# Kernel optimization log

Measured on AMD Instinct MI355X. Metric: run time of the kernel, lower is better.

The kernel has to match this reference:

```python
import jax, jax.numpy as jnp
import numpy as np

B, N, C, K = 4, 4096, 128, 16
LN_EPS = 1e-5


def knn(x, k):
    # x: [B,N,3] -> idx of k nearest (incl. self): [B,N,k]
    xx = jnp.sum(x * x, axis=2, keepdims=True)            # [B,N,1]
    inner = -2.0 * jnp.matmul(x, jnp.swapaxes(x, 1, 2))   # [B,N,N]
    pairwise = -xx - inner - jnp.swapaxes(xx, 1, 2)       # = -||xi-xj||^2
    _, idx = jax.lax.top_k(pairwise, k)                   # largest = nearest
    return idx


def index_points(points, idx):
    # points: [B,N,C], idx: [B,N,K] -> [B,N,K,C]
    return jax.vmap(lambda p, i: p[i])(points, idx)


def layer_norm(x, g, b):
    m = jnp.mean(x, axis=-1, keepdims=True)
    v = jnp.mean((x - m) ** 2, axis=-1, keepdims=True)
    return (x - m) * jax.lax.rsqrt(v + LN_EPS) * g + b


def setup_inputs() -> dict:
    key = jax.random.key(0)
    ks = jax.random.split(key, 16)
    h, q = C // 2, C // 4
    w = lambda k, s, sc: jax.random.normal(k, s, jnp.float32) * sc
    return dict(
        xyz=jax.random.normal(ks[0], (B, N, 3), jnp.float32),
        features=jax.random.normal(ks[1], (B, N, C), jnp.float32),
        geo_w1=w(ks[2], (10, h), 0.3), geo_b1=jnp.zeros((h,), jnp.float32),
        geo_g1=jnp.ones((h,), jnp.float32), geo_be1=jnp.zeros((h,), jnp.float32),
        geo_w2=w(ks[3], (h, h), 0.12), geo_b2=jnp.zeros((h,), jnp.float32),
        diff_w1=w(ks[4], (C, h), 0.09), diff_b1=jnp.zeros((h,), jnp.float32),
        diff_g1=jnp.ones((h,), jnp.float32), diff_be1=jnp.zeros((h,), jnp.float32),
        diff_w2=w(ks[5], (h, h), 0.12), diff_b2=jnp.zeros((h,), jnp.float32),
        ep_w1=w(ks[6], (C, q), 0.09), ep_b1=jnp.zeros((q,), jnp.float32),
        ep_w2=w(ks[7], (q, 1), 0.17), ep_b2=jnp.zeros((1,), jnp.float32),
        ref_w1=w(ks[8], (2 * C, C), 0.06), ref_b1=jnp.zeros((C,), jnp.float32),
        ref_g1=jnp.ones((C,), jnp.float32), ref_be1=jnp.zeros((C,), jnp.float32),
    )


def reference(xyz, features,
              geo_w1, geo_b1, geo_g1, geo_be1, geo_w2, geo_b2,
              diff_w1, diff_b1, diff_g1, diff_be1, diff_w2, diff_b2,
              ep_w1, ep_b1, ep_w2, ep_b2,
              ref_w1, ref_b1, ref_g1, ref_be1):
    # --- geometric features ---
    idx = knn(xyz, K)                                    # [B,N,K]
    neighbors = index_points(xyz, idx)                   # [B,N,K,3]
    rel_pos = neighbors - xyz[:, :, None, :]             # [B,N,K,3]
    cov = jnp.einsum('bnkc,bnkd->bncd', rel_pos, rel_pos) / K  # [B,N,3,3]
    _, eigvecs = jnp.linalg.eigh(cov)                    # ascending eigenvalues
    normal = eigvecs[..., :, 0]                          # smallest-eig direction
    curvature_dir = eigvecs[..., :, 2]                   # largest-eig direction
    mean_rel = jnp.mean(rel_pos, axis=2)                 # [B,N,3]
    mean_dist = jnp.mean(jnp.linalg.norm(rel_pos, axis=-1), axis=-1, keepdims=True)
    geo_feat = jnp.concatenate([normal, curvature_dir, mean_rel, mean_dist], axis=-1)  # [B,N,10]

    geo_h = layer_norm(geo_feat @ geo_w1 + geo_b1, geo_g1, geo_be1)
    geo_encoded = jax.nn.relu(geo_h) @ geo_w2 + geo_b2   # [B,N,C/2]

    # --- feature differences (knn recomputed as in the original) ---
    idx2 = knn(xyz, K)
    neighbor_feats = index_points(features, idx2)        # [B,N,K,C]
    feat_diff = jnp.mean(jnp.abs(features[:, :, None, :] - neighbor_feats), axis=2)  # [B,N,C]
    diff_h = layer_norm(feat_diff @ diff_w1 + diff_b1, diff_g1, diff_be1)
    diff_encoded = jax.nn.relu(diff_h) @ diff_w2 + diff_b2

    # --- edge probability + refinement ---
    edge_feat = jnp.concatenate([geo_encoded, diff_encoded], axis=-1)  # [B,N,C]
    ep_h = jax.nn.relu(edge_feat @ ep_w1 + ep_b1)
    edge_prob = jax.nn.sigmoid(ep_h @ ep_w2 + ep_b2)     # [B,N,1]

    enhanced = jnp.concatenate([features, edge_feat * edge_prob], axis=-1)  # [B,N,2C]
    refined = jax.nn.relu(layer_norm(enhanced @ ref_w1 + ref_b1, ref_g1, ref_be1))
    refined = refined + features                          # dropout in eval mode = identity
    return refined, edge_prob
```

## Files before the change

### kernel.cpp

```cpp
#include <hip/hip_runtime.h>
#include <hip/hip_bf16.h>

#define N_ 4096
#define C_ 128
#define K_ 16
#define NPT 16384

__device__ __forceinline__ float wave_sum64(float v) {
#pragma unroll
  for (int off = 32; off >= 1; off >>= 1) v += __shfl_xor(v, off, 64);
  return v;
}


__device__ __forceinline__ float sign_f(float a, float b) {
  return copysignf(fabsf(a), b);
}

__device__ float lapy2_f(float x, float y) {
#pragma clang fp contract(off)
  float xa = fabsf(x), ya = fabsf(y);
  float w = fmaxf(xa, ya), z = fminf(xa, ya);
  if (z == 0.0f) return w;
  float t = z / w;
  return w * sqrtf(1.0f + t * t);
}

__device__ void lartg_f(float f, float g, float& c, float& s, float& r) {
#pragma clang fp contract(off)
  if (g == 0.0f) {
    c = 1.0f; s = 0.0f; r = f;
  } else if (f == 0.0f) {
    c = 0.0f; s = copysignf(1.0f, g); r = fabsf(g);
  } else {
    float d = sqrtf(f * f + g * g);
    c = fabsf(f) / d;
    r = sign_f(d, f);
    s = g / r;
  }
}

__device__ void laev2_f(float a, float b, float cc, float& rt1, float& rt2,
                        float& cs1, float& sn1) {
#pragma clang fp contract(off)
  float sm = a + cc;
  float df = a - cc;
  float adf = fabsf(df);
  float tb = b + b;
  float ab = fabsf(tb);
  float acmx, acmn;
  if (fabsf(a) > fabsf(cc)) { acmx = a; acmn = cc; } else { acmx = cc; acmn = a; }
  float rt;
  if (adf > ab) {
    float t = ab / adf; rt = adf * sqrtf(1.0f + t * t);
  } else if (adf < ab) {
    float t = adf / ab; rt = ab * sqrtf(1.0f + t * t);
  } else {
    rt = ab * sqrtf(2.0f);
  }
  int sgn1;
  if (sm < 0.0f) {
    rt1 = 0.5f * (sm - rt); sgn1 = -1;
    rt2 = (acmx / rt1) * acmn - (b / rt1) * b;
  } else if (sm > 0.0f) {
    rt1 = 0.5f * (sm + rt); sgn1 = 1;
    rt2 = (acmx / rt1) * acmn - (b / rt1) * b;
  } else {
    rt1 = 0.5f * rt; rt2 = -0.5f * rt; sgn1 = 1;
  }
  float cs; int sgn2;
  if (df >= 0.0f) { cs = df + rt; sgn2 = 1; } else { cs = df - rt; sgn2 = -1; }
  float acs = fabsf(cs);
  if (acs > ab) {
    float ct = -tb / cs;
    sn1 = 1.0f / sqrtf(1.0f + ct * ct);
    cs1 = ct * sn1;
  } else {
    if (ab == 0.0f) { cs1 = 1.0f; sn1 = 0.0f; }
    else {
      float tn = -cs / tb;
      cs1 = 1.0f / sqrtf(1.0f + tn * tn);
      sn1 = tn * cs1;
    }
  }
  if (sgn1 == sgn2) { float tn = cs1; cs1 = -sn1; sn1 = tn; }
}

__device__ void steqr3_f(float d[3], float e[2], float Z[3][3]) {
#pragma clang fp contract(off)
  const int n = 3;
  const float eps = 5.9604644775390625e-08f;
  const float eps2 = eps * eps;
  const float safmin = 1.17549435e-38f;
  const int nmaxit = n * 30;
  int jtot = 0;
  int l1 = 1;

  for (int og = 0; og < 16; ++og) {
    if (l1 > n) break;
    if (l1 > 1) e[l1 - 2] = 0.0f;
    int m, l, lend;
    if (l1 <= n - 1) {
      bool found = false;
      for (m = l1; m <= n - 1; ++m) {
        float tst = fabsf(e[m - 1]);
        if (tst == 0.0f) { found = true; break; }
        if (tst <= (sqrtf(fabsf(d[m - 1])) * sqrtf(fabsf(d[m]))) * eps) {
          e[m - 1] = 0.0f; found = true; break;
        }
      }
      if (!found) m = n;
    } else {
      m = n;
    }
    l = l1; lend = m; l1 = m + 1;
    if (lend == l) continue;
    if (fabsf(d[lend - 1]) < fabsf(d[l - 1])) { int t = l; l = lend; lend = t; }

    if (lend > l) {
      for (int it = 0; it < 128; ++it) {
        int mm;
        if (l != lend) {
          bool f2 = false;
          for (mm = l; mm <= lend - 1; ++mm) {
            float tst = e[mm - 1] * e[mm - 1];
            if (tst <= (eps2 * fabsf(d[mm - 1])) * fabsf(d[mm]) + safmin) { f2 = true; break; }
          }
          if (!f2) mm = lend;
        } else mm = lend;
        if (mm < lend) e[mm - 1] = 0.0f;
        float p = d[l - 1];
        if (mm == l) {
          d[l - 1] = p; ++l;
          if (l <= lend) continue;
          break;
        }
        if (mm == l + 1) {
          float rt1, rt2, cc, ss;
          laev2_f(d[l - 1], e[l - 1], d[l], rt1, rt2, cc, ss);
          for (int r = 0; r < n; ++r) {
            float temp = Z[r][l];
            Z[r][l] = cc * temp - ss * Z[r][l - 1];
            Z[r][l - 1] = ss * temp + cc * Z[r][l - 1];
          }
          d[l - 1] = rt1; d[l] = rt2; e[l - 1] = 0.0f;
          l += 2;
          if (l <= lend) continue;
          break;
        }
        if (jtot == nmaxit) break;
        ++jtot;
        float g = (d[l] - p) / (2.0f * e[l - 1]);
        float r = lapy2_f(g, 1.0f);
        g = d[mm - 1] - p + e[l - 1] / (g + sign_f(r, g));
        float s = 1.0f, c = 1.0f;
        p = 0.0f;
        float csv[2], snv[2];
        for (int i = mm - 1; i >= l; --i) {
          float f = s * e[i - 1];
          float bb = c * e[i - 1];
          lartg_f(g, f, c, s, r);
          if (i != mm - 1) e[i] = r;
          g = d[i] - p;
          r = (d[i - 1] - g) * s + 2.0f * c * bb;
          p = s * r;
          d[i] = g + p;
          g = c * r - bb;
          csv[i - l] = c;
          snv[i - l] = -s;
        }
        int mml = mm - l;
        for (int j = mml; j >= 1; --j) {
          float cc = csv[j - 1], ss = snv[j - 1];
          for (int r2 = 0; r2 < n; ++r2) {
            float temp = Z[r2][l + j - 1];
            Z[r2][l + j - 1] = cc * temp - ss * Z[r2][l + j - 2];
            Z[r2][l + j - 2] = ss * temp + cc * Z[r2][l + j - 2];
          }
        }
        d[l - 1] -= p;
        e[l - 1] = g;
      }
    } else {
      for (int it = 0; it < 128; ++it) {
        int mm;
        if (l != lend) {
          bool f2 = false;
          for (mm = l; mm >= lend + 1; --mm) {
            float tst = e[mm - 2] * e[mm - 2];
            if (tst <= (eps2 * fabsf(d[mm - 1])) * fabsf(d[mm - 2]) + safmin) { f2 = true; break; }
          }
          if (!f2) mm = lend;
        } else mm = lend;
        if (mm > lend) e[mm - 2] = 0.0f;
        float p = d[l - 1];
        if (mm == l) {
          d[l - 1] = p; --l;
          if (l >= lend) continue;
          break;
        }
        if (mm == l - 1) {
          float rt1, rt2, cc, ss;
          laev2_f(d[l - 2], e[l - 2], d[l - 1], rt1, rt2, cc, ss);
          for (int r = 0; r < n; ++r) {
            float temp = Z[r][l - 1];
            Z[r][l - 1] = cc * temp - ss * Z[r][l - 2];
            Z[r][l - 2] = ss * temp + cc * Z[r][l - 2];
          }
          d[l - 2] = rt1; d[l - 1] = rt2; e[l - 2] = 0.0f;
          l -= 2;
          if (l >= lend) continue;
          break;
        }
        if (jtot == nmaxit) break;
        ++jtot;
        float g = (d[l - 2] - p) / (2.0f * e[l - 2]);
        float r = lapy2_f(g, 1.0f);
        g = d[mm - 1] - p + e[l - 2] / (g + sign_f(r, g));
        float s = 1.0f, c = 1.0f;
        p = 0.0f;
        float csv[2], snv[2];
        for (int i = mm; i <= l - 1; ++i) {
          float f = s * e[i - 1];
          float bb = c * e[i - 1];
          lartg_f(g, f, c, s, r);
          if (i != mm) e[i - 2] = r;
          g = d[i - 1] - p;
          r = (d[i] - g) * s + 2.0f * c * bb;
          p = s * r;
          d[i - 1] = g + p;
          g = c * r - bb;
          csv[i - mm] = c;
          snv[i - mm] = s;
        }
        int lm = l - mm;
        for (int j = 1; j <= lm; ++j) {
          float cc = csv[j - 1], ss = snv[j - 1];
          for (int r2 = 0; r2 < n; ++r2) {
            float temp = Z[r2][mm + j - 1];
            Z[r2][mm + j - 1] = cc * temp - ss * Z[r2][mm + j - 2];
            Z[r2][mm + j - 2] = ss * temp + cc * Z[r2][mm + j - 2];
          }
        }
        d[l - 1] -= p;
        e[l - 2] = g;
      }
    }
  }
  for (int ii = 2; ii <= n; ++ii) {
    int i = ii - 1, k = i;
    float p = d[i - 1];
    for (int j = ii; j <= n; ++j) {
      if (d[j - 1] < p) { k = j; p = d[j - 1]; }
    }
    if (k != i) {
      d[k - 1] = d[i - 1]; d[i - 1] = p;
      for (int r = 0; r < n; ++r) {
        float t = Z[r][i - 1]; Z[r][i - 1] = Z[r][k - 1]; Z[r][k - 1] = t;
      }
    }
  }
}

__device__ void eig3_f(float A00, float A10, float A20,
                       float A11, float A21, float A22, float Z[3][3]) {
#pragma clang fp contract(off)
  float d[3], e[2];
  float tau = 0.0f, v2 = 0.0f;
  d[0] = A00;
  float xnorm = fabsf(A20);
  if (xnorm == 0.0f) {
    tau = 0.0f; v2 = 0.0f;
    e[0] = A10; d[1] = A11; e[1] = A21; d[2] = A22;
  } else {
    float beta = -sign_f(lapy2_f(A10, xnorm), A10);
    tau = (beta - A10) / beta;
    float inv = 1.0f / (A10 - beta);
    v2 = A20 * inv;
    e[0] = beta;
    float x0 = tau * A11;
    float x1 = tau * A21;
    float tmp2 = A21 * v2;
    x0 = x0 + tau * tmp2;
    x1 = x1 + (tau * v2) * A22;
    float dotv = x0 + x1 * v2;
    float aw = (-0.5f * tau) * dotv;
    float w0 = x0 + aw;
    float w1 = x1 + aw * v2;
    d[1] = (A11 - w0) - w0;
    float pq = v2 * w0;
    e[1] = (A21 - pq) - w1;
    float pr = v2 * w1;
    d[2] = (A22 - pr) - pr;
  }
  Z[0][0] = 1.0f; Z[0][1] = 0.0f; Z[0][2] = 0.0f;
  Z[1][0] = 0.0f; Z[1][1] = 1.0f; Z[1][2] = 0.0f;
  Z[2][0] = 0.0f; Z[2][1] = 0.0f; Z[2][2] = 1.0f;
  steqr3_f(d, e, Z);
  if (tau != 0.0f) {
    for (int j = 0; j < 3; ++j) {
      float sum = Z[1][j] + v2 * Z[2][j];
      float tw = tau * sum;
      Z[1][j] = Z[1][j] - tw;
      Z[2][j] = Z[2][j] - v2 * tw;
    }
  }
}

__device__ __forceinline__ unsigned long long knn_key(float qx, float qy, float qz,
                                                      float nqxx, float x, float y,
                                                      float z, int j) {
  const float dot = __fmaf_rn(qz, z, __fmaf_rn(qy, y, __fmul_rn(qx, x)));
  const float xxj =
      __fadd_rn(__fadd_rn(__fmul_rn(x, x), __fmul_rn(y, y)), __fmul_rn(z, z));
  const float inner = __fmul_rn(-2.0f, dot);
  const float pval = __fsub_rn(__fsub_rn(nqxx, inner), xxj);
  const unsigned bits = __float_as_uint(pval);
  const unsigned ordv = bits ^ (unsigned)(((int)bits >> 31) | 0x80000000);
  return ((unsigned long long)ordv << 32) | (unsigned)(4095 - j);
}

__global__ __launch_bounds__(256, 6) void knn_kernel(const float* __restrict__ xyz,
                                                     int* __restrict__ nidx_ws) {
  __shared__ float4 tile4[1024];

  const int wave = threadIdx.x >> 6;
  const int lane = threadIdx.x & 63;
  const int tid = threadIdx.x;
  const int P0 = blockIdx.x * 8;
  const int b = P0 >> 12;
  const int r0 = P0 & 4095;
  const int pbase = r0 + wave * 2;
  const float* xb = xyz + (size_t)b * (N_ * 3);

  float qx[2], qy[2], qz[2], nqxx[2];
#pragma unroll
  for (int q = 0; q < 2; ++q) {
    const int i = pbase + q;
    qx[q] = xb[3 * i]; qy[q] = xb[3 * i + 1]; qz[q] = xb[3 * i + 2];
    nqxx[q] = -__fadd_rn(__fadd_rn(__fmul_rn(qx[q], qx[q]), __fmul_rn(qy[q], qy[q])),
                         __fmul_rn(qz[q], qz[q]));
  }

  unsigned long long pk[2][4];
#pragma unroll
  for (int q = 0; q < 2; ++q)
#pragma unroll
    for (int s = 0; s < 4; ++s) pk[q][s] = 0ull;

  for (int tile = 0; tile < 4; ++tile) {
    {
      const float4* gsrc = (const float4*)(xb + tile * 3072);
      float4 a0 = gsrc[tid * 3];
      float4 a1 = gsrc[tid * 3 + 1];
      float4 a2 = gsrc[tid * 3 + 2];
      const int base = tid * 4;
      tile4[base]     = make_float4(a0.x, a0.y, a0.z, 0.0f);
      tile4[base + 1] = make_float4(a0.w, a1.x, a1.y, 0.0f);
      tile4[base + 2] = make_float4(a1.z, a1.w, a2.x, 0.0f);
      tile4[base + 3] = make_float4(a2.y, a2.z, a2.w, 0.0f);
    }
    __syncthreads();

#pragma unroll 2
    for (int tloc = 0; tloc < 16; ++tloc) {
      const int idx = tloc * 64 + lane;
      const int j = tile * 1024 + idx;
      const float4 pv = tile4[idx];
      const float x = pv.x;
      const float y = pv.y;
      const float z = pv.z;
      const float xxj =
          __fadd_rn(__fadd_rn(__fmul_rn(x, x), __fmul_rn(y, y)), __fmul_rn(z, z));
      const unsigned jenc = (unsigned)(4095 - j);
#pragma unroll
      for (int q = 0; q < 2; ++q) {
        const float dot =
            __fmaf_rn(qz[q], z, __fmaf_rn(qy[q], y, __fmul_rn(qx[q], x)));
        const float inner = __fmul_rn(-2.0f, dot);
        const float pval = __fsub_rn(__fsub_rn(nqxx[q], inner), xxj);
        const unsigned bits = __float_as_uint(pval);
        const unsigned ordv = bits ^ (unsigned)(((int)bits >> 31) | 0x80000000);
        const unsigned long long key = ((unsigned long long)ordv << 32) | jenc;
        const bool c3 = key > pk[q][3];
        if (__any(c3)) {
          const bool c0 = key > pk[q][0], c1 = key > pk[q][1], c2 = key > pk[q][2];
          pk[q][3] = c3 ? (c2 ? pk[q][2] : key) : pk[q][3];
          pk[q][2] = c2 ? (c1 ? pk[q][1] : key) : pk[q][2];
          pk[q][1] = c1 ? (c0 ? pk[q][0] : key) : pk[q][1];
          pk[q][0] = c0 ? key : pk[q][0];
        }
      }
    }
    __syncthreads();
  }

  int stash[2];
  int h[2] = {0, 0};
#pragma unroll
  for (int k = 0; k < K_; ++k) {
    unsigned long long v[2];
#pragma unroll
    for (int q = 0; q < 2; ++q) v[q] = pk[q][0];
#pragma unroll
    for (int off = 32; off >= 1; off >>= 1) {
#pragma unroll
      for (int q = 0; q < 2; ++q) {
        unsigned long long ov = __shfl_xor(v[q], off, 64);
        if (ov > v[q]) v[q] = ov;
      }
    }
#pragma unroll
    for (int q = 0; q < 2; ++q) {
      const int jidx = (4095 - (int)(unsigned)(v[q] & 0xFFFFFFFFull)) & (N_ - 1);
      if (lane == k) stash[q] = jidx;
      if (pk[q][0] == v[q]) {
        pk[q][0] = pk[q][1]; pk[q][1] = pk[q][2]; pk[q][2] = pk[q][3];
        pk[q][3] = 0ull;
        ++h[q];
      }
    }
  }
#pragma unroll
  for (int q = 0; q < 2; ++q) {
    if (__ballot(h[q] >= 4) != 0ull) {
      unsigned long long qq[K_];
#pragma unroll
      for (int k = 0; k < K_; ++k) qq[k] = 0ull;
      for (int t = 0; t < 64; ++t) {
        const int j = t * 64 + lane;
        const unsigned long long key = knn_key(qx[q], qy[q], qz[q], nqxx[q],
                                               xb[3 * j], xb[3 * j + 1],
                                               xb[3 * j + 2], j);
        bool c[K_];
#pragma unroll
        for (int s = 0; s < K_; ++s) c[s] = key > qq[s];
#pragma unroll
        for (int s = K_ - 1; s >= 1; --s)
          qq[s] = c[s] ? (c[s - 1] ? qq[s - 1] : key) : qq[s];
        qq[0] = c[0] ? key : qq[0];
      }
#pragma unroll
      for (int k = 0; k < K_; ++k) {
        unsigned long long v = qq[0];
#pragma unroll
        for (int off = 32; off >= 1; off >>= 1) {
          unsigned long long ov = __shfl_xor(v, off, 64);
          if (ov > v) v = ov;
        }
        const int jidx = (4095 - (int)(unsigned)(v & 0xFFFFFFFFull)) & (N_ - 1);
        if (lane == k) stash[q] = jidx;
        if (qq[0] == v) {
#pragma unroll
          for (int s = 0; s < K_ - 1; ++s) qq[s] = qq[s + 1];
          qq[K_ - 1] = 0ull;
        }
      }
    }
  }

  if (lane < K_) {
    const int pg = P0 + wave * 2;
#pragma unroll
    for (int q = 0; q < 2; ++q)
      nidx_ws[(size_t)(pg + q) * K_ + lane] = stash[q];
  }
}

__global__ __launch_bounds__(64) void eig_kernel(const float* __restrict__ xyz,
                                                 const int* __restrict__ nidx_ws,
                                                 float* __restrict__ gf_ws) {
  const int p = blockIdx.x * 64 + threadIdx.x;
  const int b = p >> 12;
  const int i = p & 4095;
  const float* xb = xyz + (size_t)b * (N_ * 3);
  const float qx = xb[3 * i];
  const float qy = xb[3 * i + 1];
  const float qz = xb[3 * i + 2];

  int nidx[K_];
#pragma unroll
  for (int k = 0; k < K_; ++k) nidx[k] = nidx_ws[(size_t)p * K_ + k];

  float c00 = 0, c01 = 0, c02 = 0, c11 = 0, c12 = 0, c22 = 0;
  float mrx = 0, mry = 0, mrz = 0, md = 0;
#pragma unroll
  for (int k = 0; k < K_; ++k) {
    const int j = nidx[k];
    const float rx = __fsub_rn(xb[3 * j], qx);
    const float ry = __fsub_rn(xb[3 * j + 1], qy);
    const float rz = __fsub_rn(xb[3 * j + 2], qz);
    c00 = __fadd_rn(c00, __fmul_rn(rx, rx));
    c01 = __fadd_rn(c01, __fmul_rn(rx, ry));
    c02 = __fadd_rn(c02, __fmul_rn(rx, rz));
    c11 = __fadd_rn(c11, __fmul_rn(ry, ry));
    c12 = __fadd_rn(c12, __fmul_rn(ry, rz));
    c22 = __fadd_rn(c22, __fmul_rn(rz, rz));
    mrx = __fadd_rn(mrx, rx);
    mry = __fadd_rn(mry, ry);
    mrz = __fadd_rn(mrz, rz);
    const float nn = __fadd_rn(__fadd_rn(__fmul_rn(rx, rx), __fmul_rn(ry, ry)),
                               __fmul_rn(rz, rz));
    md = __fadd_rn(md, sqrtf(nn));
  }
  const float s16 = 0.0625f;
  float Z[3][3];
  eig3_f(__fmul_rn(c00, s16), __fmul_rn(c01, s16), __fmul_rn(c02, s16),
         __fmul_rn(c11, s16), __fmul_rn(c12, s16), __fmul_rn(c22, s16), Z);
  float* g = gf_ws + (size_t)p * 12;
  g[0] = Z[0][0]; g[1] = Z[1][0]; g[2] = Z[2][0];
  g[3] = Z[0][2]; g[4] = Z[1][2]; g[5] = Z[2][2];
  g[6] = __fmul_rn(mrx, s16); g[7] = __fmul_rn(mry, s16);
  g[8] = __fmul_rn(mrz, s16);
  g[9] = __fmul_rn(md, s16);
}

__global__ __launch_bounds__(256) void mlp_kernel(
    const float* __restrict__ feats, const int* __restrict__ nidx_ws,
    const float* __restrict__ gf_ws,
    const float* __restrict__ geo_w1, const float* __restrict__ geo_b1,
    const float* __restrict__ geo_g1, const float* __restrict__ geo_be1,
    const float* __restrict__ geo_w2, const float* __restrict__ geo_b2,
    const float* __restrict__ diff_w1, const float* __restrict__ diff_b1,
    const float* __restrict__ diff_g1, const float* __restrict__ diff_be1,
    const float* __restrict__ diff_w2, const float* __restrict__ diff_b2,
    const float* __restrict__ ep_w1, const float* __restrict__ ep_b1,
    const float* __restrict__ ep_w2, const float* __restrict__ ep_b2,
    const float* __restrict__ ref_w1, const float* __restrict__ ref_b1,
    const float* __restrict__ ref_g1, const float* __restrict__ ref_be1,
    float* __restrict__ out, float* __restrict__ out_prob) {

  __shared__ float w[8192];
  __shared__ float fsh[16 * 128];
  __shared__ float sdif[16 * 128];
  __shared__ float ysh[16 * 64];
  __shared__ float edsh[16 * 128];
  __shared__ float insh[16 * 12];
  __shared__ int nsh[16 * 16];

  const int tid = threadIdx.x;
  const int lane = tid & 63;
  const int g = tid >> 6;
  const int P0 = blockIdx.x * 16;
  const int b = P0 >> 12;
  const int r0 = P0 & 4095;
  const float* fb = feats + (size_t)b * N_ * C_;

  if (tid < 192) insh[tid] = gf_ws[(size_t)P0 * 12 + tid];
  nsh[tid] = nidx_ws[(size_t)P0 * K_ + tid];
#pragma unroll
  for (int m = 0; m < 8; ++m)
    fsh[m * 256 + tid] = fb[(size_t)r0 * C_ + m * 256 + tid];
  if (tid < 160) ((float4*)w)[tid] = ((const float4*)geo_w1)[tid];
#pragma unroll
  for (int m = 0; m < 4; ++m)
    ((float4*)(w + 640))[m * 256 + tid] = ((const float4*)geo_w2)[m * 256 + tid];
  __syncthreads();

  {
    float acc[4] = {0, 0, 0, 0};
#pragma unroll
    for (int c = 0; c < 10; ++c) {
      const float wv = w[c * 64 + lane];
#pragma unroll
      for (int ptl = 0; ptl < 4; ++ptl)
        acc[ptl] += insh[(g * 4 + ptl) * 12 + c] * wv;
    }
#pragma unroll
    for (int ptl = 0; ptl < 4; ++ptl) {
      const int pt = g * 4 + ptl;
      float a = acc[ptl] + geo_b1[lane];
      float m = wave_sum64(a) * (1.0f / 64.0f);
      float xm = a - m;
      float var = wave_sum64(xm * xm) * (1.0f / 64.0f);
      float yv = xm * (1.0f / sqrtf(var + 1e-5f)) * geo_g1[lane] + geo_be1[lane];
      ysh[pt * 64 + lane] = fmaxf(yv, 0.0f);
    }
  }
  __syncthreads();

  float ge[4] = {0, 0, 0, 0}, de[4], prob[4];
#pragma unroll 4
  for (int c = 0; c < 64; ++c) {
    const float wv = w[640 + c * 64 + lane];
#pragma unroll
    for (int ptl = 0; ptl < 4; ++ptl)
      ge[ptl] += ysh[(g * 4 + ptl) * 64 + c] * wv;
  }
#pragma unroll
  for (int ptl = 0; ptl < 4; ++ptl) ge[ptl] += geo_b2[lane];

  {
    const int h2 = tid >> 7, c = tid & 127;
    for (int ptp = 0; ptp < 8; ++ptp) {
      const int pt = h2 * 8 + ptp;
      const float fv = fsh[pt * 128 + c];
      float s = 0.0f;
#pragma unroll
      for (int k = 0; k < K_; ++k) {
        const int j = nsh[pt * 16 + k];
        s += fabsf(fv - fb[(size_t)j * C_ + c]);
      }
      sdif[pt * 128 + c] = s * (1.0f / 16.0f);
    }
  }
  __syncthreads();
#pragma unroll
  for (int m = 0; m < 8; ++m)
    ((float4*)w)[m * 256 + tid] = ((const float4*)diff_w1)[m * 256 + tid];
  __syncthreads();

  {
    float acc[4] = {0, 0, 0, 0};
#pragma unroll 4
    for (int c = 0; c < 128; ++c) {
      const float wv = w[c * 64 + lane];
#pragma unroll
      for (int ptl = 0; ptl < 4; ++ptl)
        acc[ptl] += sdif[(g * 4 + ptl) * 128 + c] * wv;
    }
#pragma unroll
    for (int ptl = 0; ptl < 4; ++ptl) {
      const int pt = g * 4 + ptl;
      float a = acc[ptl] + diff_b1[lane];
      float m = wave_sum64(a) * (1.0f / 64.0f);
      float xm = a - m;
      float var = wave_sum64(xm * xm) * (1.0f / 64.0f);
      float yv = xm * (1.0f / sqrtf(var + 1e-5f)) * diff_g1[lane] + diff_be1[lane];
      ysh[pt * 64 + lane] = fmaxf(yv, 0.0f);
    }
  }
  __syncthreads();
#pragma unroll
  for (int m = 0; m < 4; ++m)
    ((float4*)w)[m * 256 + tid] = ((const float4*)diff_w2)[m * 256 + tid];
#pragma unroll
  for (int m = 0; m < 4; ++m)
    ((float4*)w)[1024 + m * 256 + tid] = ((const float4*)ep_w1)[m * 256 + tid];
  __syncthreads();

  {
    float acc[4] = {0, 0, 0, 0};
#pragma unroll 4
    for (int c = 0; c < 64; ++c) {
      const float wv = w[c * 64 + lane];
#pragma unroll
      for (int ptl = 0; ptl < 4; ++ptl)
        acc[ptl] += ysh[(g * 4 + ptl) * 64 + c] * wv;
    }
#pragma unroll
    for (int ptl = 0; ptl < 4; ++ptl) {
      const int pt = g * 4 + ptl;
      de[ptl] = acc[ptl] + diff_b2[lane];
      edsh[pt * 128 + lane] = ge[ptl];
      edsh[pt * 128 + 64 + lane] = de[ptl];
    }
  }
  __syncthreads();

  const int u = lane & 31;
  {
    float ea[4] = {0, 0, 0, 0};
#pragma unroll 4
    for (int c = 0; c < 128; ++c) {
      const float wv = w[4096 + c * 32 + u];
#pragma unroll
      for (int ptl = 0; ptl < 4; ++ptl)
        ea[ptl] += edsh[(g * 4 + ptl) * 128 + c] * wv;
    }
#pragma unroll
    for (int ptl = 0; ptl < 4; ++ptl) {
      float a = ea[ptl] + ep_b1[u];
      float hh = (lane < 32) ? fmaxf(a, 0.0f) * ep_w2[u] : 0.0f;
      float tsum = wave_sum64(hh) + ep_b2[0];
      prob[ptl] = 1.0f / (1.0f + expf(-tsum));
    }
  }
  __syncthreads();
#pragma unroll
  for (int ptl = 0; ptl < 4; ++ptl) {
    const int pt = g * 4 + ptl;
    edsh[pt * 128 + lane] = ge[ptl] * prob[ptl];
    edsh[pt * 128 + 64 + lane] = de[ptl] * prob[ptl];
  }

  float a0[4] = {0, 0, 0, 0}, a1[4] = {0, 0, 0, 0};
  for (int ch = 0; ch < 4; ++ch) {
    __syncthreads();
    {
      const float4* gsrc = (const float4*)(ref_w1 + ch * 8192);
#pragma unroll
      for (int m = 0; m < 8; ++m) ((float4*)w)[m * 256 + tid] = gsrc[m * 256 + tid];
    }
    __syncthreads();
#pragma unroll 4
    for (int cl = 0; cl < 64; ++cl) {
      const float w0 = w[cl * 128 + lane];
      const float w1v = w[cl * 128 + 64 + lane];
#pragma unroll
      for (int ptl = 0; ptl < 4; ++ptl) {
        const int pt = g * 4 + ptl;
        const float e = (ch < 2) ? fsh[pt * 128 + ch * 64 + cl]
                                 : edsh[pt * 128 + (ch - 2) * 64 + cl];
        a0[ptl] += e * w0;
        a1[ptl] += e * w1v;
      }
    }
  }

#pragma unroll
  for (int ptl = 0; ptl < 4; ++ptl) {
    const int pt = g * 4 + ptl;
    float A0 = a0[ptl] + ref_b1[lane];
    float A1 = a1[ptl] + ref_b1[64 + lane];
    float mm2 = wave_sum64(A0 + A1) * (1.0f / 128.0f);
    float d0 = A0 - mm2, d1 = A1 - mm2;
    float var2 = wave_sum64(d0 * d0 + d1 * d1) * (1.0f / 128.0f);
    float rs = 1.0f / sqrtf(var2 + 1e-5f);
    float y0 = d0 * rs * ref_g1[lane] + ref_be1[lane];
    float y1 = d1 * rs * ref_g1[64 + lane] + ref_be1[64 + lane];
    y0 = fmaxf(y0, 0.0f) + fsh[pt * 128 + lane];
    y1 = fmaxf(y1, 0.0f) + fsh[pt * 128 + 64 + lane];
    out[(size_t)(P0 + pt) * 128 + lane] = y0;
    out[(size_t)(P0 + pt) * 128 + 64 + lane] = y1;
    if (lane == 0) out_prob[P0 + pt] = prob[ptl];
  }
}

__global__ __launch_bounds__(256) void fused_kernel(
    const float* __restrict__ xyz, const float* __restrict__ feats,
    const float* __restrict__ geo_w1, const float* __restrict__ geo_b1,
    const float* __restrict__ geo_g1, const float* __restrict__ geo_be1,
    const float* __restrict__ geo_w2, const float* __restrict__ geo_b2,
    const float* __restrict__ diff_w1, const float* __restrict__ diff_b1,
    const float* __restrict__ diff_g1, const float* __restrict__ diff_be1,
    const float* __restrict__ diff_w2, const float* __restrict__ diff_b2,
    const float* __restrict__ ep_w1, const float* __restrict__ ep_b1,
    const float* __restrict__ ep_w2, const float* __restrict__ ep_b2,
    const float* __restrict__ ref_w1, const float* __restrict__ ref_b1,
    const float* __restrict__ ref_g1, const float* __restrict__ ref_be1,
    float* __restrict__ out, float* __restrict__ out_prob) {

  __shared__ float4 tile4[1024];

  const int wave = threadIdx.x >> 6;
  const int lane = threadIdx.x & 63;
  const int tid = threadIdx.x;
  const int p = blockIdx.x * 4 + wave;
  const int b = p >> 12;
  const int i = p & 4095;
  const float* xb = xyz + (size_t)b * (N_ * 3);

  const float qx = xb[3 * i];
  const float qy = xb[3 * i + 1];
  const float qz = xb[3 * i + 2];
  const float qxx =
      __fadd_rn(__fadd_rn(__fmul_rn(qx, qx), __fmul_rn(qy, qy)), __fmul_rn(qz, qz));
  const float nqxx = -qxx;

  unsigned long long pk[4] = {0ull, 0ull, 0ull, 0ull};
  for (int tile = 0; tile < 4; ++tile) {
    {
      const float4* gsrc = (const float4*)(xb + tile * 3072);
      float4 r0v = gsrc[tid * 3];
      float4 r1 = gsrc[tid * 3 + 1];
      float4 r2 = gsrc[tid * 3 + 2];
      const int base = tid * 4;
      tile4[base]     = make_float4(r0v.x, r0v.y, r0v.z, 0.0f);
      tile4[base + 1] = make_float4(r0v.w, r1.x, r1.y, 0.0f);
      tile4[base + 2] = make_float4(r1.z, r1.w, r2.x, 0.0f);
      tile4[base + 3] = make_float4(r2.y, r2.z, r2.w, 0.0f);
    }
    __syncthreads();
#pragma unroll 4
    for (int tloc = 0; tloc < 16; ++tloc) {
      const int j = tile * 1024 + tloc * 64 + lane;
      const float4 pt = tile4[tloc * 64 + lane];
      const unsigned long long key = knn_key(qx, qy, qz, nqxx, pt.x, pt.y, pt.z, j);
      const bool c0 = key > pk[0], c1 = key > pk[1], c2 = key > pk[2], c3 = key > pk[3];
      pk[3] = c3 ? (c2 ? pk[2] : key) : pk[3];
      pk[2] = c2 ? (c1 ? pk[1] : key) : pk[2];
      pk[1] = c1 ? (c0 ? pk[0] : key) : pk[1];
      pk[0] = c0 ? key : pk[0];
    }
    __syncthreads();
  }

  int nidx[K_];
  int h = 0;
#pragma unroll
  for (int k = 0; k < K_; ++k) {
    unsigned long long v = pk[0];
#pragma unroll
    for (int off = 32; off >= 1; off >>= 1) {
      unsigned long long ov = __shfl_xor(v, off, 64);
      if (ov > v) v = ov;
    }
    nidx[k] = (4095 - (int)(unsigned)(v & 0xFFFFFFFFull)) & (N_ - 1);
    if (pk[0] == v) {
      pk[0] = pk[1]; pk[1] = pk[2]; pk[2] = pk[3]; pk[3] = 0ull;
      ++h;
    }
  }
  if (__ballot(h >= 4) != 0ull) {
    unsigned long long q[K_];
#pragma unroll
    for (int k = 0; k < K_; ++k) q[k] = 0ull;
    for (int t = 0; t < 64; ++t) {
      const int j = t * 64 + lane;
      const unsigned long long key =
          knn_key(qx, qy, qz, nqxx, xb[3 * j], xb[3 * j + 1], xb[3 * j + 2], j);
      bool c[K_];
#pragma unroll
      for (int s = 0; s < K_; ++s) c[s] = key > q[s];
#pragma unroll
      for (int s = K_ - 1; s >= 1; --s)
        q[s] = c[s] ? (c[s - 1] ? q[s - 1] : key) : q[s];
      q[0] = c[0] ? key : q[0];
    }
#pragma unroll
    for (int k = 0; k < K_; ++k) {
      unsigned long long v = q[0];
#pragma unroll
      for (int off = 32; off >= 1; off >>= 1) {
        unsigned long long ov = __shfl_xor(v, off, 64);
        if (ov > v) v = ov;
      }
      nidx[k] = (4095 - (int)(unsigned)(v & 0xFFFFFFFFull)) & (N_ - 1);
      if (q[0] == v) {
#pragma unroll
        for (int s = 0; s < K_ - 1; ++s) q[s] = q[s + 1];
        q[K_ - 1] = 0ull;
      }
    }
  }

  float c00 = 0, c01 = 0, c02 = 0, c11 = 0, c12 = 0, c22 = 0;
  float mrx = 0, mry = 0, mrz = 0, md = 0;
#pragma unroll
  for (int k = 0; k < K_; ++k) {
    const int j = nidx[k];
    const float rx = __fsub_rn(xb[3 * j], qx);
    const float ry = __fsub_rn(xb[3 * j + 1], qy);
    const float rz = __fsub_rn(xb[3 * j + 2], qz);
    c00 = __fadd_rn(c00, __fmul_rn(rx, rx));
    c01 = __fadd_rn(c01, __fmul_rn(rx, ry));
    c02 = __fadd_rn(c02, __fmul_rn(rx, rz));
    c11 = __fadd_rn(c11, __fmul_rn(ry, ry));
    c12 = __fadd_rn(c12, __fmul_rn(ry, rz));
    c22 = __fadd_rn(c22, __fmul_rn(rz, rz));
    mrx = __fadd_rn(mrx, rx);
    mry = __fadd_rn(mry, ry);
    mrz = __fadd_rn(mrz, rz);
    const float nn = __fadd_rn(__fadd_rn(__fmul_rn(rx, rx), __fmul_rn(ry, ry)),
                               __fmul_rn(rz, rz));
    md = __fadd_rn(md, sqrtf(nn));
  }
  const float s16 = 0.0625f;
  float Z[3][3];
  eig3_f(__fmul_rn(c00, s16), __fmul_rn(c01, s16), __fmul_rn(c02, s16),
         __fmul_rn(c11, s16), __fmul_rn(c12, s16), __fmul_rn(c22, s16), Z);
  float gf[10];
  gf[0] = Z[0][0]; gf[1] = Z[1][0]; gf[2] = Z[2][0];
  gf[3] = Z[0][2]; gf[4] = Z[1][2]; gf[5] = Z[2][2];
  gf[6] = __fmul_rn(mrx, s16); gf[7] = __fmul_rn(mry, s16);
  gf[8] = __fmul_rn(mrz, s16);
  gf[9] = __fmul_rn(md, s16);

  float acc = 0.0f;
#pragma unroll
  for (int ii = 0; ii < 10; ++ii) acc += gf[ii] * geo_w1[ii * 64 + lane];
  acc += geo_b1[lane];
  float yr;
  {
    float m = wave_sum64(acc) * (1.0f / 64.0f);
    float xm = acc - m;
    float var = wave_sum64(xm * xm) * (1.0f / 64.0f);
    float yv = xm * (1.0f / sqrtf(var + 1e-5f)) * geo_g1[lane] + geo_be1[lane];
    yr = fmaxf(yv, 0.0f);
  }
  float ge = 0.0f;
#pragma unroll 8
  for (int jj = 0; jj < 64; ++jj) ge += __shfl(yr, jj, 64) * geo_w2[jj * 64 + lane];
  ge += geo_b2[lane];

  const float* fb = feats + (size_t)b * N_ * C_;
  const float* fi = fb + (size_t)i * C_;
  const float f0 = fi[lane];
  const float f1 = fi[64 + lane];
  float s0 = 0.0f, s1 = 0.0f;
#pragma unroll
  for (int k = 0; k < K_; ++k) {
    const float* fj = fb + (size_t)nidx[k] * C_;
    s0 += fabsf(f0 - fj[lane]);
    s1 += fabsf(f1 - fj[64 + lane]);
  }
  s0 *= (1.0f / 16.0f);
  s1 *= (1.0f / 16.0f);
  float acc2 = 0.0f;
#pragma unroll 8
  for (int c = 0; c < 64; ++c) acc2 += __shfl(s0, c, 64) * diff_w1[c * 64 + lane];
#pragma unroll 8
  for (int c = 64; c < 128; ++c) acc2 += __shfl(s1, c - 64, 64) * diff_w1[c * 64 + lane];
  acc2 += diff_b1[lane];
  float yr2;
  {
    float m = wave_sum64(acc2) * (1.0f / 64.0f);
    float xm = acc2 - m;
    float var = wave_sum64(xm * xm) * (1.0f / 64.0f);
    float yv = xm * (1.0f / sqrtf(var + 1e-5f)) * diff_g1[lane] + diff_be1[lane];
    yr2 = fmaxf(yv, 0.0f);
  }
  float de = 0.0f;
#pragma unroll 8
  for (int jj = 0; jj < 64; ++jj) de += __shfl(yr2, jj, 64) * diff_w2[jj * 64 + lane];
  de += diff_b2[lane];

  {
    const int u = lane & 31;
    float a = 0.0f;
#pragma unroll 8
    for (int c = 0; c < 64; ++c) a += __shfl(ge, c, 64) * ep_w1[c * 32 + u];
#pragma unroll 8
    for (int c = 64; c < 128; ++c) a += __shfl(de, c - 64, 64) * ep_w1[c * 32 + u];
    a += ep_b1[u];
    float hh = (lane < 32) ? fmaxf(a, 0.0f) * ep_w2[u] : 0.0f;
    float tsum = wave_sum64(hh) + ep_b2[0];
    float prob = 1.0f / (1.0f + expf(-tsum));

    const float gep = ge * prob;
    const float dep = de * prob;
    float a0 = 0.0f, a1 = 0.0f;
#pragma unroll 4
    for (int c = 0; c < 64; ++c) {
      float ec = __shfl(f0, c, 64);
      a0 += ec * ref_w1[c * 128 + lane];
      a1 += ec * ref_w1[c * 128 + 64 + lane];
    }
#pragma unroll 4
    for (int c = 64; c < 128; ++c) {
      float ec = __shfl(f1, c - 64, 64);
      a0 += ec * ref_w1[c * 128 + lane];
      a1 += ec * ref_w1[c * 128 + 64 + lane];
    }
#pragma unroll 4
    for (int c = 128; c < 192; ++c) {
      float ec = __shfl(gep, c - 128, 64);
      a0 += ec * ref_w1[c * 128 + lane];
      a1 += ec * ref_w1[c * 128 + 64 + lane];
    }
#pragma unroll 4
    for (int c = 192; c < 256; ++c) {
      float ec = __shfl(dep, c - 192, 64);
      a0 += ec * ref_w1[c * 128 + lane];
      a1 += ec * ref_w1[c * 128 + 64 + lane];
    }
    a0 += ref_b1[lane];
    a1 += ref_b1[64 + lane];
    float mm2 = wave_sum64(a0 + a1) * (1.0f / 128.0f);
    float d0 = a0 - mm2, d1 = a1 - mm2;
    float var2 = wave_sum64(d0 * d0 + d1 * d1) * (1.0f / 128.0f);
    float rs = 1.0f / sqrtf(var2 + 1e-5f);
    float y0 = d0 * rs * ref_g1[lane] + ref_be1[lane];
    float y1 = d1 * rs * ref_g1[64 + lane] + ref_be1[64 + lane];
    y0 = fmaxf(y0, 0.0f) + f0;
    y1 = fmaxf(y1, 0.0f) + f1;
    out[(size_t)p * 128 + lane] = y0;
    out[(size_t)p * 128 + 64 + lane] = y1;
    if (lane == 0) out_prob[p] = prob;
  }
}

extern "C" void kernel_launch(void* const* d_in, const int* in_sizes, int n_in,
                              void* d_out, int out_size, void* d_ws, size_t ws_size,
                              hipStream_t stream) {
  const float* xyz = (const float*)d_in[0];
  const float* features = (const float*)d_in[1];
  const float* geo_w1 = (const float*)d_in[2];
  const float* geo_b1 = (const float*)d_in[3];
  const float* geo_g1 = (const float*)d_in[4];
  const float* geo_be1 = (const float*)d_in[5];
  const float* geo_w2 = (const float*)d_in[6];
  const float* geo_b2 = (const float*)d_in[7];
  const float* diff_w1 = (const float*)d_in[8];
  const float* diff_b1 = (const float*)d_in[9];
  const float* diff_g1 = (const float*)d_in[10];
  const float* diff_be1 = (const float*)d_in[11];
  const float* diff_w2 = (const float*)d_in[12];
  const float* diff_b2 = (const float*)d_in[13];
  const float* ep_w1 = (const float*)d_in[14];
  const float* ep_b1 = (const float*)d_in[15];
  const float* ep_w2 = (const float*)d_in[16];
  const float* ep_b2 = (const float*)d_in[17];
  const float* ref_w1 = (const float*)d_in[18];
  const float* ref_b1 = (const float*)d_in[19];
  const float* ref_g1 = (const float*)d_in[20];
  const float* ref_be1 = (const float*)d_in[21];

  float* out = (float*)d_out;
  float* out_prob = out + (size_t)NPT * C_;

  if (ws_size >= (size_t)(2 * 1024 * 1024)) {
    int* nidx_ws = (int*)d_ws;
    float* gf_ws = (float*)((char*)d_ws + (1u << 20));
    knn_kernel<<<dim3(NPT / 8), dim3(256), 0, stream>>>(xyz, nidx_ws);
    eig_kernel<<<dim3(NPT / 64), dim3(64), 0, stream>>>(xyz, nidx_ws, gf_ws);
    mlp_kernel<<<dim3(NPT / 16), dim3(256), 0, stream>>>(
        features, nidx_ws, gf_ws, geo_w1, geo_b1, geo_g1, geo_be1, geo_w2,
        geo_b2, diff_w1, diff_b1, diff_g1, diff_be1, diff_w2, diff_b2, ep_w1,
        ep_b1, ep_w2, ep_b2, ref_w1, ref_b1, ref_g1, ref_be1, out, out_prob);
  } else {
    fused_kernel<<<dim3(NPT / 4), dim3(256), 0, stream>>>(
        xyz, features, geo_w1, geo_b1, geo_g1, geo_be1, geo_w2, geo_b2,
        diff_w1, diff_b1, diff_g1, diff_be1, diff_w2, diff_b2, ep_w1, ep_b1,
        ep_w2, ep_b2, ref_w1, ref_b1, ref_g1, ref_be1, out, out_prob);
  }
}
```

Before: 330.5 us.

## Precompute point norms in shared tile and register-block refinement GEMV

The KNN tile now stores each point's squared norm in the unused fourth float4 slot, so the inner search loop no longer recomputes it for every query. The refinement layer is remapped so each thread computes 4 output channels for 2 points, using float4 weight and activation loads from shared memory. LayerNorm reductions move to 32-lane group shuffles. The edge-probability write moves earlier. This is meant to cut LDS traffic and redundant ALU work, in exchange for more accumulator registers.

```diff
diff --git a/kernel.cpp b/kernel.cpp
--- a/kernel.cpp
+++ b/kernel.cpp
@@ -9,6 +9,15 @@
 __device__ __forceinline__ float wave_sum64(float v) {
 #pragma unroll
   for (int off = 32; off >= 1; off >>= 1) v += __shfl_xor(v, off, 64);
+  return v;
+}
+
+__device__ __forceinline__ float grp32_sum(float v) {
+  v += __shfl_xor(v, 1, 64);
+  v += __shfl_xor(v, 2, 64);
+  v += __shfl_xor(v, 4, 64);
+  v += __shfl_xor(v, 8, 64);
+  v += __shfl_xor(v, 16, 64);
   return v;
 }
 
@@ -355,10 +364,14 @@
       float4 a1 = gsrc[tid * 3 + 1];
       float4 a2 = gsrc[tid * 3 + 2];
       const int base = tid * 4;
-      tile4[base]     = make_float4(a0.x, a0.y, a0.z, 0.0f);
-      tile4[base + 1] = make_float4(a0.w, a1.x, a1.y, 0.0f);
-      tile4[base + 2] = make_float4(a1.z, a1.w, a2.x, 0.0f);
-      tile4[base + 3] = make_float4(a2.y, a2.z, a2.w, 0.0f);
+      const float xx0 = __fadd_rn(__fadd_rn(__fmul_rn(a0.x, a0.x), __fmul_rn(a0.y, a0.y)), __fmul_rn(a0.z, a0.z));
+      const float xx1 = __fadd_rn(__fadd_rn(__fmul_rn(a0.w, a0.w), __fmul_rn(a1.x, a1.x)), __fmul_rn(a1.y, a1.y));
+      const float xx2 = __fadd_rn(__fadd_rn(__fmul_rn(a1.z, a1.z), __fmul_rn(a1.w, a1.w)), __fmul_rn(a2.x, a2.x));
+      const float xx3 = __fadd_rn(__fadd_rn(__fmul_rn(a2.y, a2.y), __fmul_rn(a2.z, a2.z)), __fmul_rn(a2.w, a2.w));
+      tile4[base]     = make_float4(a0.x, a0.y, a0.z, xx0);
+      tile4[base + 1] = make_float4(a0.w, a1.x, a1.y, xx1);
+      tile4[base + 2] = make_float4(a1.z, a1.w, a2.x, xx2);
+      tile4[base + 3] = make_float4(a2.y, a2.z, a2.w, xx3);
     }
     __syncthreads();
 
@@ -370,8 +383,7 @@
       const float x = pv.x;
       const float y = pv.y;
       const float z = pv.z;
-      const float xxj =
-          __fadd_rn(__fadd_rn(__fmul_rn(x, x), __fmul_rn(y, y)), __fmul_rn(z, z));
+      const float xxj = pv.w;
       const unsigned jenc = (unsigned)(4095 - j);
 #pragma unroll
       for (int q = 0; q < 2; ++q) {
@@ -674,6 +686,7 @@
       float hh = (lane < 32) ? fmaxf(a, 0.0f) * ep_w2[u] : 0.0f;
       float tsum = wave_sum64(hh) + ep_b2[0];
       prob[ptl] = 1.0f / (1.0f + expf(-tsum));
+      if (lane == 0) out_prob[P0 + g * 4 + ptl] = prob[ptl];
     }
   }
   __syncthreads();
@@ -684,7 +697,11 @@
     edsh[pt * 128 + 64 + lane] = de[ptl] * prob[ptl];
   }
 
-  float a0[4] = {0, 0, 0, 0}, a1[4] = {0, 0, 0, 0};
+  const int p2 = tid >> 5;
+  const int ptA = p2 * 2, ptB = ptA + 1;
+  const int oc4 = (tid & 31) * 4;
+  float A0 = 0, A1 = 0, A2 = 0, A3 = 0;
+  float B0 = 0, B1 = 0, B2 = 0, B3 = 0;
   for (int ch = 0; ch < 4; ++ch) {
     __syncthreads();
     {
@@ -693,37 +710,61 @@
       for (int m = 0; m < 8; ++m) ((float4*)w)[m * 256 + tid] = gsrc[m * 256 + tid];
     }
     __syncthreads();
+    const float* eA = (ch < 2) ? (fsh + ptA * 128 + ch * 64)
+                               : (edsh + ptA * 128 + (ch - 2) * 64);
+    const float* eB = (ch < 2) ? (fsh + ptB * 128 + ch * 64)
+                               : (edsh + ptB * 128 + (ch - 2) * 64);
 #pragma unroll 4
-    for (int cl = 0; cl < 64; ++cl) {
-      const float w0 = w[cl * 128 + lane];
-      const float w1v = w[cl * 128 + 64 + lane];
-#pragma unroll
-      for (int ptl = 0; ptl < 4; ++ptl) {
-        const int pt = g * 4 + ptl;
-        const float e = (ch < 2) ? fsh[pt * 128 + ch * 64 + cl]
-                                 : edsh[pt * 128 + (ch - 2) * 64 + cl];
-        a0[ptl] += e * w0;
-        a1[ptl] += e * w1v;
-      }
-    }
-  }
-
-#pragma unroll
-  for (int ptl = 0; ptl < 4; ++ptl) {
-    const int pt = g * 4 + ptl;
-    float A0 = a0[ptl] + ref_b1[lane];
-    float A1 = a1[ptl] + ref_b1[64 + lane];
-    float mm2 = wave_sum64(A0 + A1) * (1.0f / 128.0f);
-    float d0 = A0 - mm2, d1 = A1 - mm2;
-    float var2 = wave_sum64(d0 * d0 + d1 * d1) * (1.0f / 128.0f);
-    float rs = 1.0f / sqrtf(var2 + 1e-5f);
-    float y0 = d0 * rs * ref_g1[lane] + ref_be1[lane];
-    float y1 = d1 * rs * ref_g1[64 + lane] + ref_be1[64 + lane];
-    y0 = fmaxf(y0, 0.0f) + fsh[pt * 128 + lane];
-    y1 = fmaxf(y1, 0.0f) + fsh[pt * 128 + 64 + lane];
-    out[(size_t)(P0 + pt) * 128 + lane] = y0;
-    out[(size_t)(P0 + pt) * 128 + 64 + lane] = y1;
-    if (lane == 0) out_prob[P0 + pt] = prob[ptl];
+    for (int c4 = 0; c4 < 64; c4 += 4) {
+      const float4 ea = *(const float4*)(eA + c4);
+      const float4 eb = *(const float4*)(eB + c4);
+      const float4 w0 = *(const float4*)(w + (c4 + 0) * 128 + oc4);
+      const float4 w1 = *(const float4*)(w + (c4 + 1) * 128 + oc4);
+      const float4 w2 = *(const float4*)(w + (c4 + 2) * 128 + oc4);
+      const float4 w3 = *(const float4*)(w + (c4 + 3) * 128 + oc4);
+      A0 += ea.x * w0.x; A0 += ea.y * w1.x; A0 += ea.z * w2.x; A0 += ea.w * w3.x;
+      A1 += ea.x * w0.y; A1 += ea.y * w1.y; A1 += ea.z * w2.y; A1 += ea.w * w3.y;
+      A2 += ea.x * w0.z; A2 += ea.y * w1.z; A2 += ea.z * w2.z; A2 += ea.w * w3.z;
+      A3 += ea.x * w0.w; A3 += ea.y * w1.w; A3 += ea.z * w2.w; A3 += ea.w * w3.w;
+      B0 += eb.x * w0.x; B0 += eb.y * w1.x; B0 += eb.z * w2.x; B0 += eb.w * w3.x;
+      B1 += eb.x * w0.y; B1 += eb.y * w1.y; B1 += eb.z * w2.y; B1 += eb.w * w3.y;
+      B2 += eb.x * w0.z; B2 += eb.y * w1.z; B2 += eb.z * w2.z; B2 += eb.w * w3.z;
+      B3 += eb.x * w0.w; B3 += eb.y * w1.w; B3 += eb.z * w2.w; B3 += eb.w * w3.w;
+    }
+  }
+
+  {
+    const float4 rb = *(const float4*)(ref_b1 + oc4);
+    A0 += rb.x; A1 += rb.y; A2 += rb.z; A3 += rb.w;
+    B0 += rb.x; B1 += rb.y; B2 += rb.z; B3 += rb.w;
+    const float4 gg = *(const float4*)(ref_g1 + oc4);
+    const float4 be = *(const float4*)(ref_be1 + oc4);
+
+    const float mA = grp32_sum(A0 + A1 + A2 + A3) * (1.0f / 128.0f);
+    const float dA0 = A0 - mA, dA1 = A1 - mA, dA2 = A2 - mA, dA3 = A3 - mA;
+    const float vA =
+        grp32_sum(dA0 * dA0 + dA1 * dA1 + dA2 * dA2 + dA3 * dA3) * (1.0f / 128.0f);
+    const float rsA = 1.0f / sqrtf(vA + 1e-5f);
+    const float4 resA = *(const float4*)(fsh + ptA * 128 + oc4);
+    float4 yA;
+    yA.x = fmaxf(dA0 * rsA * gg.x + be.x, 0.0f) + resA.x;
+    yA.y = fmaxf(dA1 * rsA * gg.y + be.y, 0.0f) + resA.y;
+    yA.z = fmaxf(dA2 * rsA * gg.z + be.z, 0.0f) + resA.z;
+    yA.w = fmaxf(dA3 * rsA * gg.w + be.w, 0.0f) + resA.w;
+    *(float4*)(out + (size_t)(P0 + ptA) * 128 + oc4) = yA;
+
+    const float mB = grp32_sum(B0 + B1 + B2 + B3) * (1.0f / 128.0f);
+    const float dB0 = B0 - mB, dB1 = B1 - mB, dB2 = B2 - mB, dB3 = B3 - mB;
+    const float vB =
+        grp32_sum(dB0 * dB0 + dB1 * dB1 + dB2 * dB2 + dB3 * dB3) * (1.0f / 128.0f);
+    const float rsB = 1.0f / sqrtf(vB + 1e-5f);
+    const float4 resB = *(const float4*)(fsh + ptB * 128 + oc4);
+    float4 yB;
+    yB.x = fmaxf(dB0 * rsB * gg.x + be.x, 0.0f) + resB.x;
+    yB.y = fmaxf(dB1 * rsB * gg.y + be.y, 0.0f) + resB.y;
+    yB.z = fmaxf(dB2 * rsB * gg.z + be.z, 0.0f) + resB.z;
+    yB.w = fmaxf(dB3 * rsB * gg.w + be.w, 0.0f) + resB.w;
+    *(float4*)(out + (size_t)(P0 + ptB) * 128 + oc4) = yB;
   }
 }
 
```

Measured after the change: 318.5 us. 3.6% less time.
